# Optimization experiments

Measured on AMD Instinct MI355X. Metric: run time of the kernel, lower is better.

Reference implementation:

```python
import jax, jax.numpy as jnp
import numpy as np

UNITS = 4096
INPUT_DIM = 1024
N = 16384


def setup_inputs() -> dict:
    key = jax.random.key(0)
    k1, k2 = jax.random.split(key)
    inputs = jax.random.normal(k1, (N, INPUT_DIM), dtype=jnp.float32)
    # Keras 'random_normal' initializer: stddev 0.05
    w = jax.random.normal(k2, (UNITS, INPUT_DIM), dtype=jnp.float32) * 0.05
    return {"inputs": inputs, "w": w}


def reference(inputs, w):
    # Pairwise squared Euclidean distance: out[n, u] = sum_d (w[u,d] - x[n,d])^2
    x_sq = jnp.sum(inputs * inputs, axis=-1, keepdims=True)        # [N, 1]
    w_sq = jnp.sum(w * w, axis=-1)                                  # [U]
    cross = jnp.einsum("nd,ud->nu", inputs, w)                     # [N, U]
    return x_sq + w_sq[None, :] - 2.0 * cross
```

## Files before the change

kernel.cpp:

```cpp
#include <hip/hip_runtime.h>
#include <cstdint>
#include <cstddef>

#define AS1 __attribute__((address_space(1)))
#define AS3 __attribute__((address_space(3)))

typedef unsigned short u16;
typedef unsigned int u32;
typedef unsigned char u8;
typedef int i32x4 __attribute__((ext_vector_type(4)));
typedef int i32x8 __attribute__((ext_vector_type(8)));
typedef float f32x4 __attribute__((ext_vector_type(4)));

constexpr int D  = 1024;
constexpr int NS = 16384;
constexpr int US = 4096;
constexpr int BM = 128, BN = 128, BK = 128;

constexpr size_t XQ_OFF  = 0;
constexpr size_t WQ_OFF  = (size_t)NS * D;
constexpr size_t XSQ_OFF = WQ_OFF + (size_t)US * D;
constexpr size_t WSQ_OFF = XSQ_OFF + (size_t)NS * 4;

__global__ __launch_bounds__(256) void quant_sq(
    const float* __restrict__ x, const float* __restrict__ w,
    u8* __restrict__ xq, u8* __restrict__ wq,
    float* __restrict__ xsq, float* __restrict__ wsq) {
  const int lane = threadIdx.x & 63;
  const int wave = blockIdx.x * 4 + (threadIdx.x >> 6);
  const int nwaves = gridDim.x * 4;
  for (int row = wave; row < NS + US; row += nwaves) {
    const float* src; u8* qdst; float* sdst; int r; float qscale;
    if (row < NS) { src = x; qdst = xq; sdst = xsq; r = row; qscale = 1.0f; }
    else          { src = w; qdst = wq; sdst = wsq; r = row - NS; qscale = 16.0f; }
    const float4* s4 = (const float4*)(src + (size_t)r * D);
    uint4* q4 = (uint4*)(qdst + (size_t)r * D);
    float s = 0.f;
#pragma unroll
    for (int it = 0; it < 4; ++it) {
      const float4 v = s4[it * 64 + lane];
      s += v.x * v.x + v.y * v.y + v.z * v.z + v.w * v.w;
      u32 p01 = __builtin_amdgcn_cvt_pk_fp8_f32(v.x * qscale, v.y * qscale, 0, false);
      u32 w0  = __builtin_amdgcn_cvt_pk_fp8_f32(v.z * qscale, v.w * qscale, p01, true);
      if (it == 0) ((u32*)&q4[0])[0] = 0;
      ((u32*)(q4 + (it >> 2)))[0] = 0;
      ((u32*)(qdst + (size_t)r * D))[it * 64 + lane] = w0;
    }
#pragma unroll
    for (int off = 32; off; off >>= 1) s += __shfl_down(s, off, 64);
    if (lane == 0) sdst[r] = s;
  }
}

__global__ __launch_bounds__(256, 3) void dist_gemm(
    const u8* __restrict__ xq, const u8* __restrict__ wq,
    const float* __restrict__ xsq, const float* __restrict__ wsq,
    float* __restrict__ out) {
  __shared__ u8 sA[BM * BK];
  __shared__ u8 sB[BN * BK];

  const int tid = threadIdx.x;
  const int lane = tid & 63;
  const int wv = tid >> 6;
  const int wm = wv >> 1;
  const int wn = wv & 1;
  const int quad = lane >> 4;
  const int l15 = lane & 15;

  const int m0 = blockIdx.y * BM;
  const int n0 = blockIdx.x * BN;

  f32x4 acc[4][4];
#pragma unroll
  for (int mt = 0; mt < 4; ++mt)
#pragma unroll
    for (int nt = 0; nt < 4; ++nt)
      acc[mt][nt] = (f32x4){0.f, 0.f, 0.f, 0.f};

  const int srow = lane >> 3;
  const int schunk = lane & 7;

  for (int kt = 0; kt < D / BK; ++kt) {
    const int k0 = kt * BK;
    __syncthreads();
#pragma unroll
    for (int i = 0; i < 4; ++i) {
      const int g = wv + i * 4;
      const int r = g * 8 + srow;
      const int cg = schunk ^ (r & 7);
      const u8* ga = xq + (size_t)(m0 + r) * D + k0 + cg * 16;
      const u8* gb = wq + (size_t)(n0 + r) * D + k0 + cg * 16;
      __builtin_amdgcn_global_load_lds((AS1 void*)(u8*)ga, (AS3 void*)(sA + g * 1024), 16, 0, 0);
      __builtin_amdgcn_global_load_lds((AS1 void*)(u8*)gb, (AS3 void*)(sB + g * 1024), 16, 0, 0);
    }
    __syncthreads();

    i32x8 b[4];
#pragma unroll
    for (int nt = 0; nt < 4; ++nt) {
      const int n = wn * 64 + nt * 16 + l15;
      const int s = n & 7;
      const i32x4 b0 = *reinterpret_cast<const i32x4*>(sB + n * BK + ((2 * quad) ^ s) * 16);
      const i32x4 b1 = *reinterpret_cast<const i32x4*>(sB + n * BK + ((2 * quad + 1) ^ s) * 16);
      b[nt] = __builtin_shufflevector(b0, b1, 0, 1, 2, 3, 4, 5, 6, 7);
    }
#pragma unroll
    for (int mt = 0; mt < 4; ++mt) {
      const int m = wm * 64 + mt * 16 + l15;
      const int s = m & 7;
      const i32x4 a0 = *reinterpret_cast<const i32x4*>(sA + m * BK + ((2 * quad) ^ s) * 16);
      const i32x4 a1 = *reinterpret_cast<const i32x4*>(sA + m * BK + ((2 * quad + 1) ^ s) * 16);
      const i32x8 a = __builtin_shufflevector(a0, a1, 0, 1, 2, 3, 4, 5, 6, 7);
#pragma unroll
      for (int nt = 0; nt < 4; ++nt) {
        acc[mt][nt] = __builtin_amdgcn_mfma_scale_f32_16x16x128_f8f6f4(
            a, b[nt], acc[mt][nt],  0,  0,
             0, 0x7F7F7F7F,  0, 0x7F7F7F7F);
      }
    }
  }

#pragma unroll
  for (int mt = 0; mt < 4; ++mt) {
    const int R0 = m0 + wm * 64 + mt * 16 + quad * 4;
#pragma unroll
    for (int nt = 0; nt < 4; ++nt) {
      const int C = n0 + wn * 64 + nt * 16 + l15;
      const float wsv = wsq[C];
#pragma unroll
      for (int r = 0; r < 4; ++r) {
        const int R = R0 + r;
        out[(size_t)R * US + C] = xsq[R] + wsv - 0.125f * acc[mt][nt][r];
      }
    }
  }
}

extern "C" void kernel_launch(void* const* d_in, const int* in_sizes, int n_in,
                              void* d_out, int out_size, void* d_ws, size_t ws_size,
                              hipStream_t stream) {
  const float* x = (const float*)d_in[0];
  const float* w = (const float*)d_in[1];
  float* out = (float*)d_out;
  char* ws = (char*)d_ws;

  u8* xq = (u8*)(ws + XQ_OFF);
  u8* wq = (u8*)(ws + WQ_OFF);
  float* xsq = (float*)(ws + XSQ_OFF);
  float* wsq = (float*)(ws + WSQ_OFF);

  quant_sq<<<dim3(640), dim3(256), 0, stream>>>(x, w, xq, wq, xsq, wsq);
  dist_gemm<<<dim3(US / BN, NS / BM), dim3(256), 0, stream>>>(xq, wq, xsq, wsq, out);
}
```

Measured before the change: 399.7 us.

## Double-buffer LDS with 256x256 tiles and 8-wave blocks in FP8 GEMM

The distance GEMM tile grows from 128x128 to 256x256, and the block from 4 to 8 waves, each wave computing 128x64 of output. Staging is now double-buffered in 128 KB of LDS: tile kt+2 is prefetched with global_load_lds while tile kt is computed, coordinated by explicit vmcnt waits and barriers. MFMA issue is raised in priority with s_setprio. The quantize kernel also drops redundant zero stores. The large LDS footprint limits occupancy to one block per CU, so latency hiding now depends on the prefetch pipeline.

New measurement: 388.5 us. 2.8% less time.

```diff
diff --git a/kernel.cpp b/kernel.cpp
--- a/kernel.cpp
+++ b/kernel.cpp
@@ -15,7 +15,8 @@
 constexpr int D  = 1024;
 constexpr int NS = 16384;
 constexpr int US = 4096;
-constexpr int BM = 128, BN = 128, BK = 128;
+constexpr int BM = 256, BN = 256, BK = 128;
+constexpr int KT = D / BK;
 
 constexpr size_t XQ_OFF  = 0;
 constexpr size_t WQ_OFF  = (size_t)NS * D;
@@ -34,7 +35,7 @@
     if (row < NS) { src = x; qdst = xq; sdst = xsq; r = row; qscale = 1.0f; }
     else          { src = w; qdst = wq; sdst = wsq; r = row - NS; qscale = 16.0f; }
     const float4* s4 = (const float4*)(src + (size_t)r * D);
-    uint4* q4 = (uint4*)(qdst + (size_t)r * D);
+    u32* qrow = (u32*)(qdst + (size_t)r * D);
     float s = 0.f;
 #pragma unroll
     for (int it = 0; it < 4; ++it) {
@@ -42,9 +43,7 @@
       s += v.x * v.x + v.y * v.y + v.z * v.z + v.w * v.w;
       u32 p01 = __builtin_amdgcn_cvt_pk_fp8_f32(v.x * qscale, v.y * qscale, 0, false);
       u32 w0  = __builtin_amdgcn_cvt_pk_fp8_f32(v.z * qscale, v.w * qscale, p01, true);
-      if (it == 0) ((u32*)&q4[0])[0] = 0;
-      ((u32*)(q4 + (it >> 2)))[0] = 0;
-      ((u32*)(qdst + (size_t)r * D))[it * 64 + lane] = w0;
+      qrow[it * 64 + lane] = w0;
     }
 #pragma unroll
     for (int off = 32; off; off >>= 1) s += __shfl_down(s, off, 64);
@@ -52,48 +51,64 @@
   }
 }
 
-__global__ __launch_bounds__(256, 3) void dist_gemm(
+__global__ __launch_bounds__(512, 2) void dist_gemm(
     const u8* __restrict__ xq, const u8* __restrict__ wq,
     const float* __restrict__ xsq, const float* __restrict__ wsq,
     float* __restrict__ out) {
-  __shared__ u8 sA[BM * BK];
-  __shared__ u8 sB[BN * BK];
+  __shared__ u8 lds[2 * 65536];
 
   const int tid = threadIdx.x;
   const int lane = tid & 63;
   const int wv = tid >> 6;
-  const int wm = wv >> 1;
-  const int wn = wv & 1;
+  const int wm = wv >> 2;
+  const int wn = wv & 3;
   const int quad = lane >> 4;
   const int l15 = lane & 15;
 
   const int m0 = blockIdx.y * BM;
   const int n0 = blockIdx.x * BN;
 
-  f32x4 acc[4][4];
+  f32x4 acc[8][4];
 #pragma unroll
-  for (int mt = 0; mt < 4; ++mt)
+  for (int mt = 0; mt < 8; ++mt)
 #pragma unroll
     for (int nt = 0; nt < 4; ++nt)
       acc[mt][nt] = (f32x4){0.f, 0.f, 0.f, 0.f};
 
-  const int srow = lane >> 3;
-  const int schunk = lane & 7;
+  const int srow = tid >> 3;
+  const int sch = lane & 7;
 
-  for (int kt = 0; kt < D / BK; ++kt) {
+  auto stage = [&](int buf, int kt) {
+    u8* base = lds + buf * 65536;
     const int k0 = kt * BK;
-    __syncthreads();
 #pragma unroll
-    for (int i = 0; i < 4; ++i) {
-      const int g = wv + i * 4;
-      const int r = g * 8 + srow;
-      const int cg = schunk ^ (r & 7);
+    for (int s = 0; s < 4; ++s) {
+      const int r = s * 64 + srow;
+      const int cg = sch ^ (r & 7);
       const u8* ga = xq + (size_t)(m0 + r) * D + k0 + cg * 16;
+      __builtin_amdgcn_global_load_lds((AS1 void*)(u8*)ga,
+          (AS3 void*)(base + s * 8192 + wv * 1024), 16, 0, 0);
+    }
+#pragma unroll
+    for (int s = 0; s < 4; ++s) {
+      const int r = s * 64 + srow;
+      const int cg = sch ^ (r & 7);
       const u8* gb = wq + (size_t)(n0 + r) * D + k0 + cg * 16;
-      __builtin_amdgcn_global_load_lds((AS1 void*)(u8*)ga, (AS3 void*)(sA + g * 1024), 16, 0, 0);
-      __builtin_amdgcn_global_load_lds((AS1 void*)(u8*)gb, (AS3 void*)(sB + g * 1024), 16, 0, 0);
+      __builtin_amdgcn_global_load_lds((AS1 void*)(u8*)gb,
+          (AS3 void*)(base + 32768 + s * 8192 + wv * 1024), 16, 0, 0);
     }
-    __syncthreads();
+  };
+
+  stage(0, 0);
+  stage(1, 1);
+  asm volatile("s_waitcnt vmcnt(8)" ::: "memory");
+  __builtin_amdgcn_sched_barrier(0);
+  __builtin_amdgcn_s_barrier();
+  __builtin_amdgcn_sched_barrier(0);
+
+  for (int kt = 0; kt < KT; ++kt) {
+    const u8* sA = lds + (kt & 1) * 65536;
+    const u8* sB = sA + 32768;
 
     i32x8 b[4];
 #pragma unroll
@@ -105,24 +120,41 @@
       b[nt] = __builtin_shufflevector(b0, b1, 0, 1, 2, 3, 4, 5, 6, 7);
     }
 #pragma unroll
-    for (int mt = 0; mt < 4; ++mt) {
-      const int m = wm * 64 + mt * 16 + l15;
+    for (int mt = 0; mt < 8; ++mt) {
+      const int m = wm * 128 + mt * 16 + l15;
       const int s = m & 7;
       const i32x4 a0 = *reinterpret_cast<const i32x4*>(sA + m * BK + ((2 * quad) ^ s) * 16);
       const i32x4 a1 = *reinterpret_cast<const i32x4*>(sA + m * BK + ((2 * quad + 1) ^ s) * 16);
       const i32x8 a = __builtin_shufflevector(a0, a1, 0, 1, 2, 3, 4, 5, 6, 7);
+      __builtin_amdgcn_s_setprio(1);
 #pragma unroll
       for (int nt = 0; nt < 4; ++nt) {
         acc[mt][nt] = __builtin_amdgcn_mfma_scale_f32_16x16x128_f8f6f4(
             a, b[nt], acc[mt][nt],  0,  0,
              0, 0x7F7F7F7F,  0, 0x7F7F7F7F);
       }
+      __builtin_amdgcn_s_setprio(0);
     }
+
+    if (kt == KT - 1) break;
+
+    __builtin_amdgcn_sched_barrier(0);
+    __builtin_amdgcn_s_barrier();
+    __builtin_amdgcn_sched_barrier(0);
+    if (kt + 2 < KT) {
+      stage(kt & 1, kt + 2);
+      asm volatile("s_waitcnt vmcnt(8)" ::: "memory");
+    } else {
+      asm volatile("s_waitcnt vmcnt(0)" ::: "memory");
+    }
+    __builtin_amdgcn_sched_barrier(0);
+    __builtin_amdgcn_s_barrier();
+    __builtin_amdgcn_sched_barrier(0);
   }
 
 #pragma unroll
-  for (int mt = 0; mt < 4; ++mt) {
-    const int R0 = m0 + wm * 64 + mt * 16 + quad * 4;
+  for (int mt = 0; mt < 8; ++mt) {
+    const int R0 = m0 + wm * 128 + mt * 16 + quad * 4;
 #pragma unroll
     for (int nt = 0; nt < 4; ++nt) {
       const int C = n0 + wn * 64 + nt * 16 + l15;
@@ -150,5 +182,5 @@
   float* wsq = (float*)(ws + WSQ_OFF);
 
   quant_sq<<<dim3(640), dim3(256), 0, stream>>>(x, w, xq, wq, xsq, wsq);
-  dist_gemm<<<dim3(US / BN, NS / BM), dim3(256), 0, stream>>>(xq, wq, xsq, wsq, out);
+  dist_gemm<<<dim3(US / BN, NS / BM), dim3(512), 0, stream>>>(xq, wq, xsq, wsq, out);
 }
```
